# Performance work log

Hardware: AMD Instinct MI355X
Metric: run time of the kernel (lower is better)

Reference implementation:

```python
import jax, jax.numpy as jnp
import numpy as np

N = 100000   # nodes
E = 800000   # edges
D = 128      # uniform hidden width
L = 3        # number of SAGE layers (len(hidden_channels)-1)
EPS = 1e-5   # BatchNorm eps


def setup_inputs() -> dict:
    key = jax.random.key(0)
    ks = jax.random.split(key, 7)
    s = 1.0 / np.sqrt(D)
    x = jax.random.normal(ks[0], (N, D), jnp.float32)
    edge_index = jax.random.randint(ks[1], (2, E), 0, N)
    Wl = jax.random.normal(ks[2], (L, D, D), jnp.float32) * s  # neighbor-branch weight (out,in)
    Wr = jax.random.normal(ks[3], (L, D, D), jnp.float32) * s  # root-branch weight (out,in)
    b = jax.random.normal(ks[4], (L, D), jnp.float32) * 0.01   # bias (lin_l only, PyG default)
    gamma = 1.0 + 0.1 * jax.random.normal(ks[5], (L, D), jnp.float32)
    beta = 0.1 * jax.random.normal(ks[6], (L, D), jnp.float32)
    return {"x": x, "edge_index": edge_index, "Wl": Wl, "Wr": Wr, "b": b,
            "gamma": gamma, "beta": beta}


def _sage(x, src, dst, Wl, Wr, b):
    # PyG SAGEConv: out = lin_l(mean_{j->i} x_j) + lin_r(x_i)
    agg = jax.ops.segment_sum(x[src], dst, num_segments=N)          # [N, D]
    cnt = jax.ops.segment_sum(jnp.ones((src.shape[0], 1), x.dtype), dst,
                              num_segments=N)                        # [N, 1]
    agg = agg / jnp.maximum(cnt, 1.0)  # mean; isolated nodes stay 0
    return agg @ Wl.T + x @ Wr.T + b


def _bn(x, g, be):
    # BatchNorm1d over the node axis, batch statistics, biased variance
    m = jnp.mean(x, axis=0)
    v = jnp.var(x, axis=0)
    return g * (x - m) * jax.lax.rsqrt(v + EPS) + be


def reference(x, edge_index, Wl, Wr, b, gamma, beta):
    src, dst = edge_index[0], edge_index[1]
    # hidden layers: SAGEConv -> ELU -> (dropout, eval no-op) -> BatchNorm
    for i in range(L - 1):
        h = jax.nn.elu(_sage(x, src, dst, Wl[i], Wr[i], b[i]))
        x = _bn(h, gamma[i], beta[i])
    # final layer: SAGEConv -> BatchNorm (no ELU/dropout)
    x = _bn(_sage(x, src, dst, Wl[L - 1], Wr[L - 1], b[L - 1]), gamma[L - 1], beta[L - 1])
    return x
```

## Files before the change

kernel.cpp:

```cpp
#include <hip/hip_runtime.h>
#include <hip/hip_bf16.h>

#define N_NODES 100000
#define N_EDGES 800000
#define DD 128
#define TILE 32
#define NBLK 3125
#define NSCAN1 391
#define EPSV 1e-5f
#define ECAP 768

typedef short bf16x8 __attribute__((ext_vector_type(8)));
typedef float f32x4 __attribute__((ext_vector_type(4)));

__device__ __forceinline__ short f2bf(float f) {
    unsigned u = __float_as_uint(f);
    unsigned r = (u + 0x7fffu + ((u >> 16) & 1u)) >> 16;
    return (short)r;
}
__device__ __forceinline__ float bf2f(short s) {
    return __uint_as_float(((unsigned)(unsigned short)s) << 16);
}

__global__ void k_setup(const float* __restrict__ x, short* __restrict__ xbf,
                        const int* __restrict__ dst, int* __restrict__ cnt) {
    int i = blockIdx.x * 256 + threadIdx.x;
    if (i < N_NODES * DD / 8) {
        f32x4 v0 = *(const f32x4*)(x + (size_t)i * 8);
        f32x4 v1 = *(const f32x4*)(x + (size_t)i * 8 + 4);
        bf16x8 t;
        t[0] = f2bf(v0.x); t[1] = f2bf(v0.y); t[2] = f2bf(v0.z); t[3] = f2bf(v0.w);
        t[4] = f2bf(v1.x); t[5] = f2bf(v1.y); t[6] = f2bf(v1.z); t[7] = f2bf(v1.w);
        *(bf16x8*)&xbf[(size_t)i * 8] = t;
    }
    if (i < N_EDGES) atomicAdd(&cnt[dst[i]], 1);
}

__global__ void k_scan1(const int* __restrict__ cnt, int* __restrict__ off,
                        int* __restrict__ bsums) {
    __shared__ int s[256];
    int i = blockIdx.x * 256 + threadIdx.x;
    int t = threadIdx.x;
    s[t] = (i < N_NODES) ? cnt[i] : 0;
    __syncthreads();
    for (int d = 1; d < 256; d <<= 1) {
        int x = 0;
        if (t >= d) x = s[t - d];
        __syncthreads();
        s[t] += x;
        __syncthreads();
    }
    if (i < N_NODES) off[i + 1] = s[t];
    if (t == 255) bsums[blockIdx.x] = s[255];
}

__global__ void k_scan2(int* __restrict__ bsums) {
    __shared__ int s[512];
    int t = threadIdx.x;
    s[t] = (t < NSCAN1) ? bsums[t] : 0;
    __syncthreads();
    for (int d = 1; d < 512; d <<= 1) {
        int x = 0;
        if (t >= d) x = s[t - d];
        __syncthreads();
        s[t] += x;
        __syncthreads();
    }
    if (t < NSCAN1) bsums[t] = s[t];
}

__global__ void k_scan3(int* __restrict__ off, const int* __restrict__ bsums) {
    int i = blockIdx.x * 256 + threadIdx.x;
    int add = (blockIdx.x > 0) ? bsums[blockIdx.x - 1] : 0;
    if (i < N_NODES) off[i + 1] += add;
    if (i == 0) off[0] = 0;
}

__global__ void k_fill(const int* __restrict__ src, const int* __restrict__ dst,
                       const int* __restrict__ off, int* __restrict__ cur,
                       int* __restrict__ elist) {
    int e = blockIdx.x * 256 + threadIdx.x;
    if (e < N_EDGES) {
        int d = dst[e];
        int p = atomicSub(&cur[d], 1);
        elist[off[d] + p - 1] = src[e];
    }
}

__global__ void k_fold(const float* __restrict__ wl, const float* __restrict__ wr,
                       const float* __restrict__ b, const float* __restrict__ aff,
                       int use_aff,
                       short* __restrict__ wblo, short* __restrict__ wbro,
                       float* __restrict__ bias_base, float* __restrict__ bias_deg) {
    int o = blockIdx.x;
    int k = threadIdx.x;
    float a = use_aff ? aff[k] : 1.f;
    float c = use_aff ? aff[128 + k] : 0.f;
    float vl = wl[o * DD + k], vr = wr[o * DD + k];
    wblo[o * DD + k] = f2bf(vl * a);
    wbro[o * DD + k] = f2bf(vr * a);
    __shared__ float s1[128], s2[128];
    s1[k] = c * vr; s2[k] = c * vl;
    __syncthreads();
    for (int d = 64; d > 0; d >>= 1) {
        if (k < d) { s1[k] += s1[k + d]; s2[k] += s2[k + d]; }
        __syncthreads();
    }
    if (k == 0) {
        bias_base[o] = b[o] + s1[0];
        bias_deg[o] = s2[0];
    }
}

template <bool ELU_ON>
__global__ __launch_bounds__(256, 8) void k_sage(
    const short* __restrict__ xbf,
    const int* __restrict__ off, const int* __restrict__ elist,
    const short* __restrict__ wl, const short* __restrict__ wr,
    const float* __restrict__ bias_base, const float* __restrict__ bias_deg,
    short* __restrict__ hout, float* __restrict__ partials)
{
    __shared__ short agg_t[TILE * 128];
    __shared__ float sstat[4 * 128];
    __shared__ int soff[TILE + 1];
    __shared__ int eidx[ECAP];
    const int tid = threadIdx.x;
    const int wu = __builtin_amdgcn_readfirstlane(tid >> 6);
    const int l = tid & 63;
    const int base = blockIdx.x * TILE;
    const int qw = l >> 4;
    const int ll = l & 15;

    if (tid < TILE + 1) soff[tid] = off[min(base + tid, N_NODES)];
    __syncthreads();
    const int ebase = soff[0];
    const int etot = soff[TILE] - ebase;
    const bool ovf = etot > ECAP;
    for (int k = tid; k < (ovf ? 0 : etot); k += 256) eidx[k] = elist[ebase + k];
    __syncthreads();
    const int* ep = ovf ? (elist + ebase) : (const int*)eidx;

#pragma unroll
    for (int q = 0; q < 2; ++q) {
        const int m = wu * 8 + q * 4 + qw;
        const int ea = soff[m] - ebase;
        const int eA = soff[m + 1] - ebase;
        const int deg = eA - ea;
        float acc[8];
#pragma unroll
        for (int j = 0; j < 8; ++j) acc[j] = 0.f;

        bf16x8 v0{}, v1{}, v2{}, v3{};
        int e = ea;
#define GLOAD(sn) (*(const bf16x8*)(xbf + (size_t)(sn) * DD + 8 * ll))
        if (e < eA)     v0 = GLOAD(ep[e]);
        if (e + 1 < eA) v1 = GLOAD(ep[e + 1]);
        if (e + 2 < eA) v2 = GLOAD(ep[e + 2]);
        if (e + 3 < eA) v3 = GLOAD(ep[e + 3]);
        while (__any((int)(e < eA))) {
            if (e < eA) {
#pragma unroll
                for (int j = 0; j < 8; ++j) acc[j] += bf2f(v0[j]);
                if (e + 4 < eA) v0 = GLOAD(ep[e + 4]);
            }
            if (e + 1 < eA) {
#pragma unroll
                for (int j = 0; j < 8; ++j) acc[j] += bf2f(v1[j]);
                if (e + 5 < eA) v1 = GLOAD(ep[e + 5]);
            }
            if (e + 2 < eA) {
#pragma unroll
                for (int j = 0; j < 8; ++j) acc[j] += bf2f(v2[j]);
                if (e + 6 < eA) v2 = GLOAD(ep[e + 6]);
            }
            if (e + 3 < eA) {
#pragma unroll
                for (int j = 0; j < 8; ++j) acc[j] += bf2f(v3[j]);
                if (e + 7 < eA) v3 = GLOAD(ep[e + 7]);
            }
            e += 4;
        }
#undef GLOAD

        float inv = deg > 0 ? 1.f / (float)deg : 0.f;
        bf16x8 t;
#pragma unroll
        for (int j = 0; j < 8; ++j) t[j] = f2bf(acc[j] * inv);
        *(bf16x8*)&agg_t[m * DD + ((8 * ll) ^ ((m & 7) << 3))] = t;
    }
    __syncthreads();

    const int p = wu >> 1;
    const int half = wu & 1;
    f32x4 acc[4];
#pragma unroll
    for (int nb = 0; nb < 4; ++nb) acc[nb] = f32x4{0.f, 0.f, 0.f, 0.f};
    const int mrow = p * 16 + (l & 15);
    const int kg = (l >> 4) * 8;
    const int nloc = l & 15;
    const int groot = min(base + mrow, N_NODES - 1);
#pragma unroll
    for (int ks = 0; ks < 4; ++ks) {
        int kk = ks * 32 + kg;
        int sw = kk ^ ((mrow & 7) << 3);
        bf16x8 aa = *(const bf16x8*)&agg_t[mrow * DD + sw];
        bf16x8 ax = *(const bf16x8*)(xbf + (size_t)groot * DD + kk);
#pragma unroll
        for (int nb = 0; nb < 4; ++nb) {
            int n = half * 64 + nb * 16 + nloc;
            bf16x8 bl = *(const bf16x8*)&wl[n * DD + kk];
            bf16x8 br = *(const bf16x8*)&wr[n * DD + kk];
            acc[nb] = __builtin_amdgcn_mfma_f32_16x16x32_bf16(aa, bl, acc[nb], 0, 0, 0);
            acc[nb] = __builtin_amdgcn_mfma_f32_16x16x32_bf16(ax, br, acc[nb], 0, 0, 0);
        }
    }
    __syncthreads();

    int degf[4];
#pragma unroll
    for (int r = 0; r < 4; ++r) {
        int mr_ = p * 16 + (l >> 4) * 4 + r;
        degf[r] = soff[mr_ + 1] - soff[mr_];
    }

    float colS[4], colQ[4];
#pragma unroll
    for (int nb = 0; nb < 4; ++nb) {
        int n = half * 64 + nb * 16 + nloc;
        float bb = bias_base[n];
        float bd = bias_deg[n];
        float cs = 0.f, cq = 0.f;
#pragma unroll
        for (int r = 0; r < 4; ++r) {
            int m = p * 16 + (l >> 4) * 4 + r;
            int g = base + m;
            float hv = acc[nb][r] + bb + (degf[r] > 0 ? bd : 0.f);
            if (ELU_ON) hv = hv > 0.f ? hv : expm1f(hv);
            agg_t[m * DD + (n ^ ((m & 7) << 3))] = f2bf(hv);
            float hm = (g < N_NODES) ? hv : 0.f;
            cs += hm;
            cq += hm * hm;
        }
        colS[nb] = cs; colQ[nb] = cq;
    }
#pragma unroll
    for (int nb = 0; nb < 4; ++nb) {
        colS[nb] += __shfl_xor(colS[nb], 16, 64);
        colS[nb] += __shfl_xor(colS[nb], 32, 64);
        colQ[nb] += __shfl_xor(colQ[nb], 16, 64);
        colQ[nb] += __shfl_xor(colQ[nb], 32, 64);
    }
    if (l < 16) {
#pragma unroll
        for (int nb = 0; nb < 4; ++nb) {
            sstat[wu * 128 + nb * 16 + l]      = colS[nb];
            sstat[wu * 128 + 64 + nb * 16 + l] = colQ[nb];
        }
    }
    __syncthreads();

#pragma unroll
    for (int k = 0; k < 2; ++k) {
        int idx = (k * 256 + tid) * 8;
        int m = idx >> 7, c = idx & 127;
        int g = base + m;
        if (g < N_NODES) {
            bf16x8 v = *(const bf16x8*)&agg_t[m * DD + (c ^ ((m & 7) << 3))];
            *(bf16x8*)&hout[(size_t)g * DD + c] = v;
        }
    }
    {
        int f = tid & 127;
        int part = tid >> 7;
        int hsel = f >> 6;
        int cw = part * 64 + (f & 63);
        float v = 0.f;
#pragma unroll
        for (int pr = 0; pr < 2; ++pr) v += sstat[(2 * pr + hsel) * 128 + cw];
        partials[blockIdx.x * 256 + tid] = v;
    }
}

__global__ void k_reduce(const float* __restrict__ partials,
                         const float* __restrict__ gamma, const float* __restrict__ beta,
                         float* __restrict__ aff) {
    int f = blockIdx.x;
    int t = threadIdx.x;
    float s = 0.f, q = 0.f;
    for (int i = t; i < NBLK; i += 256) {
        s += partials[i * 256 + f];
        q += partials[i * 256 + 128 + f];
    }
    __shared__ float rs[256], rq[256];
    rs[t] = s; rq[t] = q;
    __syncthreads();
    for (int d = 128; d > 0; d >>= 1) {
        if (t < d) { rs[t] += rs[t + d]; rq[t] += rq[t + d]; }
        __syncthreads();
    }
    if (t == 0) {
        float mean = rs[0] / (float)N_NODES;
        float var = rq[0] / (float)N_NODES - mean * mean;
        float a = gamma[f] * rsqrtf(var + EPSV);
        aff[f] = a;
        aff[128 + f] = beta[f] - mean * a;
    }
}

__global__ void k_apply(const short* __restrict__ hin, const float* __restrict__ aff,
                        float* __restrict__ out) {
    int i = blockIdx.x * 256 + threadIdx.x;
    if (i < N_NODES * DD / 8) {
        bf16x8 v = *(const bf16x8*)(hin + (size_t)i * 8);
        int f = (i * 8) & 127;
        f32x4 a0 = *(const f32x4*)(aff + f);
        f32x4 a1 = *(const f32x4*)(aff + f + 4);
        f32x4 c0 = *(const f32x4*)(aff + 128 + f);
        f32x4 c1 = *(const f32x4*)(aff + 128 + f + 4);
        f32x4 o0, o1;
        o0.x = bf2f(v[0]) * a0.x + c0.x; o0.y = bf2f(v[1]) * a0.y + c0.y;
        o0.z = bf2f(v[2]) * a0.z + c0.z; o0.w = bf2f(v[3]) * a0.w + c0.w;
        o1.x = bf2f(v[4]) * a1.x + c1.x; o1.y = bf2f(v[5]) * a1.y + c1.y;
        o1.z = bf2f(v[6]) * a1.z + c1.z; o1.w = bf2f(v[7]) * a1.w + c1.w;
        *(f32x4*)(out + (size_t)i * 8) = o0;
        *(f32x4*)(out + (size_t)i * 8 + 4) = o1;
    }
}

extern "C" void kernel_launch(void* const* d_in, const int* in_sizes, int n_in,
                              void* d_out, int out_size, void* d_ws, size_t ws_size,
                              hipStream_t stream) {
    const float* x     = (const float*)d_in[0];
    const int*   ei    = (const int*)d_in[1];
    const float* Wl    = (const float*)d_in[2];
    const float* Wr    = (const float*)d_in[3];
    const float* b     = (const float*)d_in[4];
    const float* gamma = (const float*)d_in[5];
    const float* beta  = (const float*)d_in[6];
    float* out = (float*)d_out;

    char* ws = (char*)d_ws;
    int*   off      = (int*)(ws + 0);
    int*   cnt      = (int*)(ws + 400128);
    int*   elist    = (int*)(ws + 800256);
    int*   bsums    = (int*)(ws + 4000256);
    float* partials = (float*)(ws + 4002304);
    float* affine   = (float*)(ws + 7202304);
    short* wbl      = (short*)(ws + 7203328);
    short* wbr      = (short*)(ws + 7236096);
    float* biasb    = (float*)(ws + 7268864);
    float* biasd    = (float*)(ws + 7269376);
    short* bufA     = (short*)(ws + 7269888);
    short* bufB     = (short*)(ws + 32869888);

    const int* src = ei;
    const int* dst = ei + N_EDGES;

    hipMemsetAsync(cnt, 0, N_NODES * sizeof(int), stream);
    k_setup<<<(N_NODES * DD / 8 + 255) / 256, 256, 0, stream>>>(x, bufA, dst, cnt);
    k_scan1<<<NSCAN1, 256, 0, stream>>>(cnt, off, bsums);
    k_scan2<<<1, 512, 0, stream>>>(bsums);
    k_scan3<<<NSCAN1, 256, 0, stream>>>(off, bsums);
    k_fill<<<(N_EDGES + 255) / 256, 256, 0, stream>>>(src, dst, off, cnt, elist);

    k_fold<<<128, 128, 0, stream>>>(Wl, Wr, b, affine, 0, wbl, wbr, biasb, biasd);
    k_sage<true><<<NBLK, 256, 0, stream>>>(bufA, off, elist, wbl, wbr,
                                           biasb, biasd, bufB, partials);
    k_reduce<<<128, 256, 0, stream>>>(partials, gamma, beta, affine);

    k_fold<<<128, 128, 0, stream>>>(Wl + DD * DD, Wr + DD * DD, b + DD, affine, 1,
                                    wbl, wbr, biasb, biasd);
    k_sage<true><<<NBLK, 256, 0, stream>>>(bufB, off, elist, wbl, wbr,
                                           biasb, biasd, bufA, partials);
    k_reduce<<<128, 256, 0, stream>>>(partials, gamma + DD, beta + DD, affine);

    k_fold<<<128, 128, 0, stream>>>(Wl + 2 * DD * DD, Wr + 2 * DD * DD, b + 2 * DD,
                                    affine, 1, wbl, wbr, biasb, biasd);
    k_sage<false><<<NBLK, 256, 0, stream>>>(bufA, off, elist, wbl, wbr,
                                            biasb, biasd, bufB, partials);
    k_reduce<<<128, 256, 0, stream>>>(partials, gamma + 2 * DD, beta + 2 * DD, affine);

    k_apply<<<(N_NODES * DD / 8 + 255) / 256, 256, 0, stream>>>(bufB, affine, out);
}
```

Before: 408.6 us.

## Make SAGE kernel persistent with atomic dynamic tile scheduling

Launches a fixed grid of 2048 blocks for each SAGE layer instead of one block per 32-node tile. Each block loops, taking the next tile from a global atomic counter. A separate zeroed counter is kept per layer, placed right after the degree-count array and cleared by the existing memset. The aim is to balance uneven per-tile edge work and cut block launch and setup overhead, at the cost of one atomic and one extra barrier per tile.

Result: slower. 630.5 us (+54.3%).

```diff
diff --git a/kernel.cpp b/kernel.cpp
--- a/kernel.cpp
+++ b/kernel.cpp
@@ -9,6 +9,7 @@
 #define NSCAN1 391
 #define EPSV 1e-5f
 #define ECAP 768
+#define PGRID 2048
 
 typedef short bf16x8 __attribute__((ext_vector_type(8)));
 typedef float f32x4 __attribute__((ext_vector_type(4)));
@@ -118,166 +119,175 @@
     const int* __restrict__ off, const int* __restrict__ elist,
     const short* __restrict__ wl, const short* __restrict__ wr,
     const float* __restrict__ bias_base, const float* __restrict__ bias_deg,
-    short* __restrict__ hout, float* __restrict__ partials)
+    short* __restrict__ hout, float* __restrict__ partials,
+    int* __restrict__ tctr)
 {
     __shared__ short agg_t[TILE * 128];
     __shared__ float sstat[4 * 128];
     __shared__ int soff[TILE + 1];
     __shared__ int eidx[ECAP];
+    __shared__ int stile;
     const int tid = threadIdx.x;
     const int wu = __builtin_amdgcn_readfirstlane(tid >> 6);
     const int l = tid & 63;
-    const int base = blockIdx.x * TILE;
     const int qw = l >> 4;
     const int ll = l & 15;
 
-    if (tid < TILE + 1) soff[tid] = off[min(base + tid, N_NODES)];
-    __syncthreads();
-    const int ebase = soff[0];
-    const int etot = soff[TILE] - ebase;
-    const bool ovf = etot > ECAP;
-    for (int k = tid; k < (ovf ? 0 : etot); k += 256) eidx[k] = elist[ebase + k];
-    __syncthreads();
-    const int* ep = ovf ? (elist + ebase) : (const int*)eidx;
-
-#pragma unroll
-    for (int q = 0; q < 2; ++q) {
-        const int m = wu * 8 + q * 4 + qw;
-        const int ea = soff[m] - ebase;
-        const int eA = soff[m + 1] - ebase;
-        const int deg = eA - ea;
-        float acc[8];
-#pragma unroll
-        for (int j = 0; j < 8; ++j) acc[j] = 0.f;
-
-        bf16x8 v0{}, v1{}, v2{}, v3{};
-        int e = ea;
+    for (;;) {
+        if (tid == 0) stile = atomicAdd(tctr, 1);
+        __syncthreads();
+        const int tile = stile;
+        if (tile >= NBLK) break;
+        const int base = tile * TILE;
+
+        if (tid < TILE + 1) soff[tid] = off[min(base + tid, N_NODES)];
+        __syncthreads();
+        const int ebase = soff[0];
+        const int etot = soff[TILE] - ebase;
+        const bool ovf = etot > ECAP;
+        for (int k = tid; k < (ovf ? 0 : etot); k += 256) eidx[k] = elist[ebase + k];
+        __syncthreads();
+        const int* ep = ovf ? (elist + ebase) : (const int*)eidx;
+
+#pragma unroll
+        for (int q = 0; q < 2; ++q) {
+            const int m = wu * 8 + q * 4 + qw;
+            const int ea = soff[m] - ebase;
+            const int eA = soff[m + 1] - ebase;
+            const int deg = eA - ea;
+            float acc[8];
+#pragma unroll
+            for (int j = 0; j < 8; ++j) acc[j] = 0.f;
+
+            bf16x8 v0{}, v1{}, v2{}, v3{};
+            int e = ea;
 #define GLOAD(sn) (*(const bf16x8*)(xbf + (size_t)(sn) * DD + 8 * ll))
-        if (e < eA)     v0 = GLOAD(ep[e]);
-        if (e + 1 < eA) v1 = GLOAD(ep[e + 1]);
-        if (e + 2 < eA) v2 = GLOAD(ep[e + 2]);
-        if (e + 3 < eA) v3 = GLOAD(ep[e + 3]);
-        while (__any((int)(e < eA))) {
-            if (e < eA) {
-#pragma unroll
-                for (int j = 0; j < 8; ++j) acc[j] += bf2f(v0[j]);
-                if (e + 4 < eA) v0 = GLOAD(ep[e + 4]);
-            }
-            if (e + 1 < eA) {
-#pragma unroll
-                for (int j = 0; j < 8; ++j) acc[j] += bf2f(v1[j]);
-                if (e + 5 < eA) v1 = GLOAD(ep[e + 5]);
-            }
-            if (e + 2 < eA) {
-#pragma unroll
-                for (int j = 0; j < 8; ++j) acc[j] += bf2f(v2[j]);
-                if (e + 6 < eA) v2 = GLOAD(ep[e + 6]);
-            }
-            if (e + 3 < eA) {
-#pragma unroll
-                for (int j = 0; j < 8; ++j) acc[j] += bf2f(v3[j]);
-                if (e + 7 < eA) v3 = GLOAD(ep[e + 7]);
-            }
-            e += 4;
-        }
+            if (e < eA)     v0 = GLOAD(ep[e]);
+            if (e + 1 < eA) v1 = GLOAD(ep[e + 1]);
+            if (e + 2 < eA) v2 = GLOAD(ep[e + 2]);
+            if (e + 3 < eA) v3 = GLOAD(ep[e + 3]);
+            while (__any((int)(e < eA))) {
+                if (e < eA) {
+#pragma unroll
+                    for (int j = 0; j < 8; ++j) acc[j] += bf2f(v0[j]);
+                    if (e + 4 < eA) v0 = GLOAD(ep[e + 4]);
+                }
+                if (e + 1 < eA) {
+#pragma unroll
+                    for (int j = 0; j < 8; ++j) acc[j] += bf2f(v1[j]);
+                    if (e + 5 < eA) v1 = GLOAD(ep[e + 5]);
+                }
+                if (e + 2 < eA) {
+#pragma unroll
+                    for (int j = 0; j < 8; ++j) acc[j] += bf2f(v2[j]);
+                    if (e + 6 < eA) v2 = GLOAD(ep[e + 6]);
+                }
+                if (e + 3 < eA) {
+#pragma unroll
+                    for (int j = 0; j < 8; ++j) acc[j] += bf2f(v3[j]);
+                    if (e + 7 < eA) v3 = GLOAD(ep[e + 7]);
+                }
+                e += 4;
+            }
 #undef GLOAD
 
-        float inv = deg > 0 ? 1.f / (float)deg : 0.f;
-        bf16x8 t;
-#pragma unroll
-        for (int j = 0; j < 8; ++j) t[j] = f2bf(acc[j] * inv);
-        *(bf16x8*)&agg_t[m * DD + ((8 * ll) ^ ((m & 7) << 3))] = t;
-    }
-    __syncthreads();
-
-    const int p = wu >> 1;
-    const int half = wu & 1;
-    f32x4 acc[4];
-#pragma unroll
-    for (int nb = 0; nb < 4; ++nb) acc[nb] = f32x4{0.f, 0.f, 0.f, 0.f};
-    const int mrow = p * 16 + (l & 15);
-    const int kg = (l >> 4) * 8;
-    const int nloc = l & 15;
-    const int groot = min(base + mrow, N_NODES - 1);
-#pragma unroll
-    for (int ks = 0; ks < 4; ++ks) {
-        int kk = ks * 32 + kg;
-        int sw = kk ^ ((mrow & 7) << 3);
-        bf16x8 aa = *(const bf16x8*)&agg_t[mrow * DD + sw];
-        bf16x8 ax = *(const bf16x8*)(xbf + (size_t)groot * DD + kk);
+            float inv = deg > 0 ? 1.f / (float)deg : 0.f;
+            bf16x8 t;
+#pragma unroll
+            for (int j = 0; j < 8; ++j) t[j] = f2bf(acc[j] * inv);
+            *(bf16x8*)&agg_t[m * DD + ((8 * ll) ^ ((m & 7) << 3))] = t;
+        }
+        __syncthreads();
+
+        const int p = wu >> 1;
+        const int half = wu & 1;
+        f32x4 acc[4];
+#pragma unroll
+        for (int nb = 0; nb < 4; ++nb) acc[nb] = f32x4{0.f, 0.f, 0.f, 0.f};
+        const int mrow = p * 16 + (l & 15);
+        const int kg = (l >> 4) * 8;
+        const int nloc = l & 15;
+        const int groot = min(base + mrow, N_NODES - 1);
+#pragma unroll
+        for (int ks = 0; ks < 4; ++ks) {
+            int kk = ks * 32 + kg;
+            int sw = kk ^ ((mrow & 7) << 3);
+            bf16x8 aa = *(const bf16x8*)&agg_t[mrow * DD + sw];
+            bf16x8 ax = *(const bf16x8*)(xbf + (size_t)groot * DD + kk);
+#pragma unroll
+            for (int nb = 0; nb < 4; ++nb) {
+                int n = half * 64 + nb * 16 + nloc;
+                bf16x8 bl = *(const bf16x8*)&wl[n * DD + kk];
+                bf16x8 br = *(const bf16x8*)&wr[n * DD + kk];
+                acc[nb] = __builtin_amdgcn_mfma_f32_16x16x32_bf16(aa, bl, acc[nb], 0, 0, 0);
+                acc[nb] = __builtin_amdgcn_mfma_f32_16x16x32_bf16(ax, br, acc[nb], 0, 0, 0);
+            }
+        }
+        __syncthreads();
+
+        int degf[4];
+#pragma unroll
+        for (int r = 0; r < 4; ++r) {
+            int mr_ = p * 16 + (l >> 4) * 4 + r;
+            degf[r] = soff[mr_ + 1] - soff[mr_];
+        }
+
+        float colS[4], colQ[4];
 #pragma unroll
         for (int nb = 0; nb < 4; ++nb) {
             int n = half * 64 + nb * 16 + nloc;
-            bf16x8 bl = *(const bf16x8*)&wl[n * DD + kk];
-            bf16x8 br = *(const bf16x8*)&wr[n * DD + kk];
-            acc[nb] = __builtin_amdgcn_mfma_f32_16x16x32_bf16(aa, bl, acc[nb], 0, 0, 0);
-            acc[nb] = __builtin_amdgcn_mfma_f32_16x16x32_bf16(ax, br, acc[nb], 0, 0, 0);
-        }
-    }
-    __syncthreads();
-
-    int degf[4];
-#pragma unroll
-    for (int r = 0; r < 4; ++r) {
-        int mr_ = p * 16 + (l >> 4) * 4 + r;
-        degf[r] = soff[mr_ + 1] - soff[mr_];
-    }
-
-    float colS[4], colQ[4];
-#pragma unroll
-    for (int nb = 0; nb < 4; ++nb) {
-        int n = half * 64 + nb * 16 + nloc;
-        float bb = bias_base[n];
-        float bd = bias_deg[n];
-        float cs = 0.f, cq = 0.f;
-#pragma unroll
-        for (int r = 0; r < 4; ++r) {
-            int m = p * 16 + (l >> 4) * 4 + r;
+            float bb = bias_base[n];
+            float bd = bias_deg[n];
+            float cs = 0.f, cq = 0.f;
+#pragma unroll
+            for (int r = 0; r < 4; ++r) {
+                int m = p * 16 + (l >> 4) * 4 + r;
+                int g = base + m;
+                float hv = acc[nb][r] + bb + (degf[r] > 0 ? bd : 0.f);
+                if (ELU_ON) hv = hv > 0.f ? hv : expm1f(hv);
+                agg_t[m * DD + (n ^ ((m & 7) << 3))] = f2bf(hv);
+                float hm = (g < N_NODES) ? hv : 0.f;
+                cs += hm;
+                cq += hm * hm;
+            }
+            colS[nb] = cs; colQ[nb] = cq;
+        }
+#pragma unroll
+        for (int nb = 0; nb < 4; ++nb) {
+            colS[nb] += __shfl_xor(colS[nb], 16, 64);
+            colS[nb] += __shfl_xor(colS[nb], 32, 64);
+            colQ[nb] += __shfl_xor(colQ[nb], 16, 64);
+            colQ[nb] += __shfl_xor(colQ[nb], 32, 64);
+        }
+        if (l < 16) {
+#pragma unroll
+            for (int nb = 0; nb < 4; ++nb) {
+                sstat[wu * 128 + nb * 16 + l]      = colS[nb];
+                sstat[wu * 128 + 64 + nb * 16 + l] = colQ[nb];
+            }
+        }
+        __syncthreads();
+
+#pragma unroll
+        for (int k = 0; k < 2; ++k) {
+            int idx = (k * 256 + tid) * 8;
+            int m = idx >> 7, c = idx & 127;
             int g = base + m;
-            float hv = acc[nb][r] + bb + (degf[r] > 0 ? bd : 0.f);
-            if (ELU_ON) hv = hv > 0.f ? hv : expm1f(hv);
-            agg_t[m * DD + (n ^ ((m & 7) << 3))] = f2bf(hv);
-            float hm = (g < N_NODES) ? hv : 0.f;
-            cs += hm;
-            cq += hm * hm;
-        }
-        colS[nb] = cs; colQ[nb] = cq;
-    }
-#pragma unroll
-    for (int nb = 0; nb < 4; ++nb) {
-        colS[nb] += __shfl_xor(colS[nb], 16, 64);
-        colS[nb] += __shfl_xor(colS[nb], 32, 64);
-        colQ[nb] += __shfl_xor(colQ[nb], 16, 64);
-        colQ[nb] += __shfl_xor(colQ[nb], 32, 64);
-    }
-    if (l < 16) {
-#pragma unroll
-        for (int nb = 0; nb < 4; ++nb) {
-            sstat[wu * 128 + nb * 16 + l]      = colS[nb];
-            sstat[wu * 128 + 64 + nb * 16 + l] = colQ[nb];
-        }
-    }
-    __syncthreads();
-
-#pragma unroll
-    for (int k = 0; k < 2; ++k) {
-        int idx = (k * 256 + tid) * 8;
-        int m = idx >> 7, c = idx & 127;
-        int g = base + m;
-        if (g < N_NODES) {
-            bf16x8 v = *(const bf16x8*)&agg_t[m * DD + (c ^ ((m & 7) << 3))];
-            *(bf16x8*)&hout[(size_t)g * DD + c] = v;
-        }
-    }
-    {
-        int f = tid & 127;
-        int part = tid >> 7;
-        int hsel = f >> 6;
-        int cw = part * 64 + (f & 63);
-        float v = 0.f;
-#pragma unroll
-        for (int pr = 0; pr < 2; ++pr) v += sstat[(2 * pr + hsel) * 128 + cw];
-        partials[blockIdx.x * 256 + tid] = v;
+            if (g < N_NODES) {
+                bf16x8 v = *(const bf16x8*)&agg_t[m * DD + (c ^ ((m & 7) << 3))];
+                *(bf16x8*)&hout[(size_t)g * DD + c] = v;
+            }
+        }
+        {
+            int f = tid & 127;
+            int part = tid >> 7;
+            int hsel = f >> 6;
+            int cw = part * 64 + (f & 63);
+            float v = 0.f;
+#pragma unroll
+            for (int pr = 0; pr < 2; ++pr) v += sstat[(2 * pr + hsel) * 128 + cw];
+            partials[tile * 256 + tid] = v;
+        }
     }
 }
 
@@ -352,11 +362,12 @@
     float* biasd    = (float*)(ws + 7269376);
     short* bufA     = (short*)(ws + 7269888);
     short* bufB     = (short*)(ws + 32869888);
+    int*   tctr     = cnt + N_NODES;
 
     const int* src = ei;
     const int* dst = ei + N_EDGES;
 
-    hipMemsetAsync(cnt, 0, N_NODES * sizeof(int), stream);
+    hipMemsetAsync(cnt, 0, (N_NODES + 3) * sizeof(int), stream);
     k_setup<<<(N_NODES * DD / 8 + 255) / 256, 256, 0, stream>>>(x, bufA, dst, cnt);
     k_scan1<<<NSCAN1, 256, 0, stream>>>(cnt, off, bsums);
     k_scan2<<<1, 512, 0, stream>>>(bsums);
@@ -364,20 +375,20 @@
     k_fill<<<(N_EDGES + 255) / 256, 256, 0, stream>>>(src, dst, off, cnt, elist);
 
     k_fold<<<128, 128, 0, stream>>>(Wl, Wr, b, affine, 0, wbl, wbr, biasb, biasd);
-    k_sage<true><<<NBLK, 256, 0, stream>>>(bufA, off, elist, wbl, wbr,
-                                           biasb, biasd, bufB, partials);
+    k_sage<true><<<PGRID, 256, 0, stream>>>(bufA, off, elist, wbl, wbr,
+                                            biasb, biasd, bufB, partials, tctr);
     k_reduce<<<128, 256, 0, stream>>>(partials, gamma, beta, affine);
 
     k_fold<<<128, 128, 0, stream>>>(Wl + DD * DD, Wr + DD * DD, b + DD, affine, 1,
                                     wbl, wbr, biasb, biasd);
-    k_sage<true><<<NBLK, 256, 0, stream>>>(bufB, off, elist, wbl, wbr,
-                                           biasb, biasd, bufA, partials);
+    k_sage<true><<<PGRID, 256, 0, stream>>>(bufB, off, elist, wbl, wbr,
+                                            biasb, biasd, bufA, partials, tctr + 1);
     k_reduce<<<128, 256, 0, stream>>>(partials, gamma + DD, beta + DD, affine);
 
     k_fold<<<128, 128, 0, stream>>>(Wl + 2 * DD * DD, Wr + 2 * DD * DD, b + 2 * DD,
                                     affine, 1, wbl, wbr, biasb, biasd);
-    k_sage<false><<<NBLK, 256, 0, stream>>>(bufA, off, elist, wbl, wbr,
-                                            biasb, biasd, bufB, partials);
+    k_sage<false><<<PGRID, 256, 0, stream>>>(bufA, off, elist, wbl, wbr,
+                                             biasb, biasd, bufB, partials, tctr + 2);
     k_reduce<<<128, 256, 0, stream>>>(partials, gamma + 2 * DD, beta + 2 * DD, affine);
 
     k_apply<<<(N_NODES * DD / 8 + 255) / 256, 256, 0, stream>>>(bufB, affine, out);
```

## Quantize gathered neighbor features to 8-bit with per-row scales

Applied to the files above, without the earlier changes.

Node features used in the neighbor gather are stored as 8-bit offset-quantized values with one float scale per 128-wide row. They are produced in setup and in the epilogue of each SAGE layer. Aggregation dequantizes on the fly by accumulating scale-weighted bytes and subtracting the offset sum, which roughly halves the bytes fetched per edge. The bf16 copy is kept for the root branch and written in place. The cost is extra quantization work, scratch reuse of the output and count buffers for the scales, and added rounding error in the aggregated features.

Result: no change. 404.7 us (median of 3 runs) (-1.0%).

```diff
diff --git a/kernel.cpp b/kernel.cpp
--- a/kernel.cpp
+++ b/kernel.cpp
@@ -23,15 +23,37 @@
 }
 
 __global__ void k_setup(const float* __restrict__ x, short* __restrict__ xbf,
+                        unsigned char* __restrict__ xq, float* __restrict__ xsc,
                         const int* __restrict__ dst, int* __restrict__ cnt) {
     int i = blockIdx.x * 256 + threadIdx.x;
     if (i < N_NODES * DD / 8) {
         f32x4 v0 = *(const f32x4*)(x + (size_t)i * 8);
         f32x4 v1 = *(const f32x4*)(x + (size_t)i * 8 + 4);
+        float f[8] = {v0.x, v0.y, v0.z, v0.w, v1.x, v1.y, v1.z, v1.w};
         bf16x8 t;
-        t[0] = f2bf(v0.x); t[1] = f2bf(v0.y); t[2] = f2bf(v0.z); t[3] = f2bf(v0.w);
-        t[4] = f2bf(v1.x); t[5] = f2bf(v1.y); t[6] = f2bf(v1.z); t[7] = f2bf(v1.w);
+#pragma unroll
+        for (int j = 0; j < 8; ++j) t[j] = f2bf(f[j]);
         *(bf16x8*)&xbf[(size_t)i * 8] = t;
+
+        float mx = 0.f;
+#pragma unroll
+        for (int j = 0; j < 8; ++j) mx = fmaxf(mx, fabsf(f[j]));
+        mx = fmaxf(mx, __shfl_xor(mx, 1, 64));
+        mx = fmaxf(mx, __shfl_xor(mx, 2, 64));
+        mx = fmaxf(mx, __shfl_xor(mx, 4, 64));
+        mx = fmaxf(mx, __shfl_xor(mx, 8, 64));
+        float qi = mx > 0.f ? 127.f / mx : 0.f;
+        unsigned w0 = 0, w1 = 0;
+#pragma unroll
+        for (int j = 0; j < 8; ++j) {
+            int u = (int)rintf(f[j] * qi) + 128;
+            u = min(max(u, 0), 255);
+            if (j < 4) w0 |= (unsigned)u << (8 * j);
+            else       w1 |= (unsigned)u << (8 * (j - 4));
+        }
+        uint2 pk; pk.x = w0; pk.y = w1;
+        *(uint2*)&xq[(size_t)i * 8] = pk;
+        if ((i & 15) == 0) xsc[i >> 4] = mx / 127.f;
     }
     if (i < N_EDGES) atomicAdd(&cnt[dst[i]], 1);
 }
@@ -112,13 +134,17 @@
     }
 }
 
-template <bool ELU_ON>
+template <bool ELU_ON, bool WQ>
 __global__ __launch_bounds__(256, 8) void k_sage(
-    const short* __restrict__ xbf,
+    short* __restrict__ xb,
+    const unsigned char* __restrict__ gq,
+    const float* __restrict__ gsc,
+    unsigned char* __restrict__ hq,
+    float* __restrict__ hsc,
     const int* __restrict__ off, const int* __restrict__ elist,
     const short* __restrict__ wl, const short* __restrict__ wr,
     const float* __restrict__ bias_base, const float* __restrict__ bias_deg,
-    short* __restrict__ hout, float* __restrict__ partials)
+    float* __restrict__ partials)
 {
     __shared__ short agg_t[TILE * 128];
     __shared__ float sstat[4 * 128];
@@ -147,45 +173,53 @@
         const int eA = soff[m + 1] - ebase;
         const int deg = eA - ea;
         float acc[8];
+        float ssum = 0.f;
 #pragma unroll
         for (int j = 0; j < 8; ++j) acc[j] = 0.f;
 
-        bf16x8 v0{}, v1{}, v2{}, v3{};
+        uint2 v0{}, v1{}, v2{}, v3{};
+        float s0f = 0.f, s1f = 0.f, s2f = 0.f, s3f = 0.f;
         int e = ea;
-#define GLOAD(sn) (*(const bf16x8*)(xbf + (size_t)(sn) * DD + 8 * ll))
-        if (e < eA)     v0 = GLOAD(ep[e]);
-        if (e + 1 < eA) v1 = GLOAD(ep[e + 1]);
-        if (e + 2 < eA) v2 = GLOAD(ep[e + 2]);
-        if (e + 3 < eA) v3 = GLOAD(ep[e + 3]);
+#define GLOAD(sn) (*(const uint2*)(gq + (size_t)(sn) * DD + 8 * ll))
+#define ACC(v, s) { ssum += (s); \
+        acc[0] += (s) * (float)((v).x & 0xffu); \
+        acc[1] += (s) * (float)(((v).x >> 8) & 0xffu); \
+        acc[2] += (s) * (float)(((v).x >> 16) & 0xffu); \
+        acc[3] += (s) * (float)((v).x >> 24); \
+        acc[4] += (s) * (float)((v).y & 0xffu); \
+        acc[5] += (s) * (float)(((v).y >> 8) & 0xffu); \
+        acc[6] += (s) * (float)(((v).y >> 16) & 0xffu); \
+        acc[7] += (s) * (float)((v).y >> 24); }
+        if (e < eA)     { int sn = ep[e];     v0 = GLOAD(sn); s0f = gsc[sn]; }
+        if (e + 1 < eA) { int sn = ep[e + 1]; v1 = GLOAD(sn); s1f = gsc[sn]; }
+        if (e + 2 < eA) { int sn = ep[e + 2]; v2 = GLOAD(sn); s2f = gsc[sn]; }
+        if (e + 3 < eA) { int sn = ep[e + 3]; v3 = GLOAD(sn); s3f = gsc[sn]; }
         while (__any((int)(e < eA))) {
             if (e < eA) {
-#pragma unroll
-                for (int j = 0; j < 8; ++j) acc[j] += bf2f(v0[j]);
-                if (e + 4 < eA) v0 = GLOAD(ep[e + 4]);
+                ACC(v0, s0f)
+                if (e + 4 < eA) { int sn = ep[e + 4]; v0 = GLOAD(sn); s0f = gsc[sn]; }
             }
             if (e + 1 < eA) {
-#pragma unroll
-                for (int j = 0; j < 8; ++j) acc[j] += bf2f(v1[j]);
-                if (e + 5 < eA) v1 = GLOAD(ep[e + 5]);
+                ACC(v1, s1f)
+                if (e + 5 < eA) { int sn = ep[e + 5]; v1 = GLOAD(sn); s1f = gsc[sn]; }
             }
             if (e + 2 < eA) {
-#pragma unroll
-                for (int j = 0; j < 8; ++j) acc[j] += bf2f(v2[j]);
-                if (e + 6 < eA) v2 = GLOAD(ep[e + 6]);
+                ACC(v2, s2f)
+                if (e + 6 < eA) { int sn = ep[e + 6]; v2 = GLOAD(sn); s2f = gsc[sn]; }
             }
             if (e + 3 < eA) {
-#pragma unroll
-                for (int j = 0; j < 8; ++j) acc[j] += bf2f(v3[j]);
-                if (e + 7 < eA) v3 = GLOAD(ep[e + 7]);
+                ACC(v3, s3f)
+                if (e + 7 < eA) { int sn = ep[e + 7]; v3 = GLOAD(sn); s3f = gsc[sn]; }
             }
             e += 4;
         }
+#undef ACC
 #undef GLOAD
 
         float inv = deg > 0 ? 1.f / (float)deg : 0.f;
         bf16x8 t;
 #pragma unroll
-        for (int j = 0; j < 8; ++j) t[j] = f2bf(acc[j] * inv);
+        for (int j = 0; j < 8; ++j) t[j] = f2bf((acc[j] - 128.f * ssum) * inv);
         *(bf16x8*)&agg_t[m * DD + ((8 * ll) ^ ((m & 7) << 3))] = t;
     }
     __syncthreads();
@@ -204,7 +238,7 @@
         int kk = ks * 32 + kg;
         int sw = kk ^ ((mrow & 7) << 3);
         bf16x8 aa = *(const bf16x8*)&agg_t[mrow * DD + sw];
-        bf16x8 ax = *(const bf16x8*)(xbf + (size_t)groot * DD + kk);
+        bf16x8 ax = *(const bf16x8*)(xb + (size_t)groot * DD + kk);
 #pragma unroll
         for (int nb = 0; nb < 4; ++nb) {
             int n = half * 64 + nb * 16 + nloc;
@@ -264,9 +298,31 @@
         int idx = (k * 256 + tid) * 8;
         int m = idx >> 7, c = idx & 127;
         int g = base + m;
-        if (g < N_NODES) {
-            bf16x8 v = *(const bf16x8*)&agg_t[m * DD + (c ^ ((m & 7) << 3))];
-            *(bf16x8*)&hout[(size_t)g * DD + c] = v;
+        bf16x8 v = *(const bf16x8*)&agg_t[m * DD + (c ^ ((m & 7) << 3))];
+        *(bf16x8*)&xb[(size_t)g * DD + c] = v;
+        if (WQ) {
+            float f[8];
+#pragma unroll
+            for (int j = 0; j < 8; ++j) f[j] = bf2f(v[j]);
+            float mx = 0.f;
+#pragma unroll
+            for (int j = 0; j < 8; ++j) mx = fmaxf(mx, fabsf(f[j]));
+            mx = fmaxf(mx, __shfl_xor(mx, 1, 64));
+            mx = fmaxf(mx, __shfl_xor(mx, 2, 64));
+            mx = fmaxf(mx, __shfl_xor(mx, 4, 64));
+            mx = fmaxf(mx, __shfl_xor(mx, 8, 64));
+            float qi = mx > 0.f ? 127.f / mx : 0.f;
+            unsigned w0 = 0, w1 = 0;
+#pragma unroll
+            for (int j = 0; j < 8; ++j) {
+                int u = (int)rintf(f[j] * qi) + 128;
+                u = min(max(u, 0), 255);
+                if (j < 4) w0 |= (unsigned)u << (8 * j);
+                else       w1 |= (unsigned)u << (8 * (j - 4));
+            }
+            uint2 pk; pk.x = w0; pk.y = w1;
+            *(uint2*)&hq[(size_t)g * DD + c] = pk;
+            if ((tid & 15) == 0) hsc[g] = mx / 127.f;
         }
     }
     {
@@ -350,35 +406,38 @@
     short* wbr      = (short*)(ws + 7236096);
     float* biasb    = (float*)(ws + 7268864);
     float* biasd    = (float*)(ws + 7269376);
-    short* bufA     = (short*)(ws + 7269888);
-    short* bufB     = (short*)(ws + 32869888);
+    short* xb       = (short*)(ws + 7269888);
+    unsigned char* qA = (unsigned char*)(ws + 32869888);
+    unsigned char* qB = (unsigned char*)(ws + 45669888);
+    float* scA = (float*)d_out;
+    float* scB = (float*)cnt;
 
     const int* src = ei;
     const int* dst = ei + N_EDGES;
 
     hipMemsetAsync(cnt, 0, N_NODES * sizeof(int), stream);
-    k_setup<<<(N_NODES * DD / 8 + 255) / 256, 256, 0, stream>>>(x, bufA, dst, cnt);
+    k_setup<<<(N_NODES * DD / 8 + 255) / 256, 256, 0, stream>>>(x, xb, qA, scA, dst, cnt);
     k_scan1<<<NSCAN1, 256, 0, stream>>>(cnt, off, bsums);
     k_scan2<<<1, 512, 0, stream>>>(bsums);
     k_scan3<<<NSCAN1, 256, 0, stream>>>(off, bsums);
     k_fill<<<(N_EDGES + 255) / 256, 256, 0, stream>>>(src, dst, off, cnt, elist);
 
     k_fold<<<128, 128, 0, stream>>>(Wl, Wr, b, affine, 0, wbl, wbr, biasb, biasd);
-    k_sage<true><<<NBLK, 256, 0, stream>>>(bufA, off, elist, wbl, wbr,
-                                           biasb, biasd, bufB, partials);
+    k_sage<true, true><<<NBLK, 256, 0, stream>>>(xb, qA, scA, qB, scB, off, elist,
+                                                 wbl, wbr, biasb, biasd, partials);
     k_reduce<<<128, 256, 0, stream>>>(partials, gamma, beta, affine);
 
     k_fold<<<128, 128, 0, stream>>>(Wl + DD * DD, Wr + DD * DD, b + DD, affine, 1,
                                     wbl, wbr, biasb, biasd);
-    k_sage<true><<<NBLK, 256, 0, stream>>>(bufB, off, elist, wbl, wbr,
-                                           biasb, biasd, bufA, partials);
+    k_sage<true, true><<<NBLK, 256, 0, stream>>>(xb, qB, scB, qA, scA, off, elist,
+                                                 wbl, wbr, biasb, biasd, partials);
     k_reduce<<<128, 256, 0, stream>>>(partials, gamma + DD, beta + DD, affine);
 
     k_fold<<<128, 128, 0, stream>>>(Wl + 2 * DD * DD, Wr + 2 * DD * DD, b + 2 * DD,
                                     affine, 1, wbl, wbr, biasb, biasd);
-    k_sage<false><<<NBLK, 256, 0, stream>>>(bufA, off, elist, wbl, wbr,
-                                            biasb, biasd, bufB, partials);
+    k_sage<false, false><<<NBLK, 256, 0, stream>>>(xb, qA, scA, qB, scB, off, elist,
+                                                   wbl, wbr, biasb, biasd, partials);
     k_reduce<<<128, 256, 0, stream>>>(partials, gamma + 2 * DD, beta + 2 * DD, affine);
 
-    k_apply<<<(N_NODES * DD / 8 + 255) / 256, 256, 0, stream>>>(bufB, affine, out);
-}
+    k_apply<<<(N_NODES * DD / 8 + 255) / 256, 256, 0, stream>>>(xb, affine, out);
+}
```
